# Optimization experiments

Hardware: AMD Instinct MI355X
Metric: run time of the kernel (lower is better)

## Reference

```python
import jax, jax.numpy as jnp
import numpy as np

B, S, H, D = 8, 1024, 16, 64
W = H * D  # hidden width = 1024


def setup_inputs() -> dict:
    key = jax.random.key(0)
    ks = jax.random.split(key, 5)
    std = 0.02
    return {
        "from_tensor": jax.random.normal(ks[0], (B, S, W), dtype=jnp.float32),
        "to_tensor": jax.random.normal(ks[1], (B, S, W), dtype=jnp.float32),
        "Wq": jax.random.normal(ks[2], (W, W), dtype=jnp.float32) * std,
        "bq": jnp.zeros((W,), dtype=jnp.float32),
        "Wk": jax.random.normal(ks[3], (W, W), dtype=jnp.float32) * std,
        "bk": jnp.zeros((W,), dtype=jnp.float32),
        "Wv": jax.random.normal(ks[4], (W, W), dtype=jnp.float32) * std,
        "bv": jnp.zeros((W,), dtype=jnp.float32),
    }


def reference(from_tensor, to_tensor, Wq, bq, Wk, bk, Wv, bv):
    # Q/K/V projections (no activations: query_act=key_act=value_act=None)
    q = from_tensor @ Wq + bq  # [B, S, W]
    k = to_tensor @ Wk + bk
    v = to_tensor @ Wv + bv
    # split heads -> [B, H, S, D]
    q = q.reshape(B, S, H, D).transpose(0, 2, 1, 3)
    k = k.reshape(B, S, H, D).transpose(0, 2, 1, 3)
    v = v.reshape(B, S, H, D).transpose(0, 2, 1, 3)
    scale = 1.0 / np.sqrt(float(D))
    scores = jnp.einsum("bhqd,bhkd->bhqk", q, k) * scale  # [B, H, S, S]
    # attention_mask=None, dropout_prob=0.0 -> no mask, no dropout
    probs = jax.nn.softmax(scores, axis=-1)
    ctx = jnp.einsum("bhqk,bhkd->bhqd", probs, v)  # [B, H, S, D]
    # merge heads -> [B, S, H*D] (do_return_2d_tensor=False)
    return ctx.transpose(0, 2, 1, 3).reshape(B, S, H * D)
```

## Files before the change

### kernel.cpp

```cpp
#include <hip/hip_runtime.h>
#include <hip/hip_bf16.h>
#include <math.h>


#define B_ 8
#define S_ 1024
#define H_ 16
#define D_ 64
#define W_ 1024

typedef __bf16 bf16x8 __attribute__((ext_vector_type(8)));
typedef float f32x4 __attribute__((ext_vector_type(4)));
typedef unsigned short ushort_t;

#define MFMA16(a, b, c) __builtin_amdgcn_mfma_f32_16x16x32_bf16((a), (b), (c), 0, 0, 0)

__device__ inline ushort_t f2bf(float f) {
    unsigned int u = __float_as_uint(f);
    u += 0x7fff + ((u >> 16) & 1);
    return (ushort_t)(u >> 16);
}

__device__ inline unsigned f2bf_rhu_u(float f) {
    return (__float_as_uint(f) + 0x8000u) >> 16;
}

__device__ inline void async16(const void* g, void* l) {
    __builtin_amdgcn_global_load_lds((const __attribute__((address_space(1))) void*)g,
                                     (__attribute__((address_space(3))) void*)l, 16, 0, 0);
}

__global__ __launch_bounds__(256) void cast2_bf16(const float* __restrict__ a,
                                                  const float* __restrict__ b,
                                                  ushort_t* __restrict__ da,
                                                  ushort_t* __restrict__ db, int n4) {
    int i = blockIdx.x * 256 + threadIdx.x;
    if (i >= n4) return;
    const float* src = blockIdx.y ? b : a;
    ushort_t* dst = blockIdx.y ? db : da;
    float4 v = ((const float4*)src)[i];
    ushort4 o;
    o.x = f2bf(v.x); o.y = f2bf(v.y); o.z = f2bf(v.z); o.w = f2bf(v.w);
    ((ushort4*)dst)[i] = o;
}

__global__ __launch_bounds__(256) void transpose_cast(const float* __restrict__ Wq,
                                                      const float* __restrict__ Wk,
                                                      const float* __restrict__ Wv,
                                                      ushort_t* __restrict__ Wt) {
    __shared__ float tile[32][33];
    int z = blockIdx.z;
    const float* src = (z == 0) ? Wq : (z == 1 ? Wk : Wv);
    ushort_t* dst = Wt + (size_t)z * W_ * W_;
    int tx = threadIdx.x, ty = threadIdx.y;
    int x = blockIdx.x * 32 + tx;
#pragma unroll
    for (int jj = 0; jj < 4; jj++) {
        int y = blockIdx.y * 32 + ty + jj * 8;
        tile[ty + jj * 8][tx] = src[(size_t)y * W_ + x];
    }
    __syncthreads();
    int x2 = blockIdx.y * 32 + tx;
#pragma unroll
    for (int jj = 0; jj < 4; jj++) {
        int y2 = blockIdx.x * 32 + ty + jj * 8;
        dst[(size_t)y2 * W_ + x2] = f2bf(tile[tx][ty + jj * 8]);
    }
}

__global__ __launch_bounds__(256) void qkv_gemm(const ushort_t* __restrict__ fromB,
                                                const ushort_t* __restrict__ toB,
                                                const ushort_t* __restrict__ Wt,
                                                const float* __restrict__ bq,
                                                const float* __restrict__ bk,
                                                const float* __restrict__ bv,
                                                ushort_t* __restrict__ Qd,
                                                ushort_t* __restrict__ Kd,
                                                ushort_t* __restrict__ Vt) {
    __shared__ __attribute__((aligned(16))) ushort_t As[128 * 32];
    __shared__ __attribute__((aligned(16))) ushort_t Bs[128 * 32];
    int z = blockIdx.y;
    const ushort_t* A = (z == 0) ? fromB : toB;
    const ushort_t* Bt = Wt + (size_t)z * (W_ * W_);
    const float* bias = (z == 0) ? bq : (z == 1 ? bk : bv);
    ushort_t* dst = (z == 0) ? Qd : (z == 1 ? Kd : Vt);

    int bx = blockIdx.x;
    int j64 = bx >> 3;
    int mTile = ((bx & 7) << 3) | (j64 >> 3);
    int nTile = j64 & 7;
    int mBase = mTile * 128, nBase = nTile * 128;

    int t = threadIdx.x;
    int lane = t & 63, w = t >> 6;
    int wm = w >> 1, wn = w & 1;
    int ln = lane & 15, qd = lane >> 4;
    int wb = t & ~63;
    int sG = ((t & 3) ^ ((t >> 3) & 3)) << 3;
    int fs = (qd ^ ((ln >> 1) & 3)) << 3;

    f32x4 zero = {0.f, 0.f, 0.f, 0.f};
    f32x4 acc[4][4];
#pragma unroll
    for (int i = 0; i < 4; i++)
#pragma unroll
        for (int j = 0; j < 4; j++) acc[i][j] = zero;

    for (int kt = 0; kt < 32; ++kt) {
        int k0 = kt * 32;
#pragma unroll
        for (int c = 0; c < 2; ++c) {
            int idx16 = c * 256 + t;
            int row = idx16 >> 2;
            async16(A + (size_t)(mBase + row) * W_ + k0 + sG, As + (size_t)(c * 256 + wb) * 8);
            async16(Bt + (size_t)(nBase + row) * W_ + k0 + sG, Bs + (size_t)(c * 256 + wb) * 8);
        }
        __syncthreads();
        bf16x8 af[4], bfr[4];
#pragma unroll
        for (int i = 0; i < 4; i++) af[i] = *(const bf16x8*)(As + (wm * 64 + i * 16 + ln) * 32 + fs);
#pragma unroll
        for (int j = 0; j < 4; j++) bfr[j] = *(const bf16x8*)(Bs + (wn * 64 + j * 16 + ln) * 32 + fs);
#pragma unroll
        for (int i = 0; i < 4; i++)
#pragma unroll
            for (int j = 0; j < 4; j++) acc[i][j] = MFMA16(af[i], bfr[j], acc[i][j]);
        __syncthreads();
    }

#pragma unroll
    for (int j = 0; j < 4; j++) {
        int n = nBase + wn * 64 + j * 16 + ln;
        float bb = bias[n];
        int h = n >> 6, d = n & 63;
#pragma unroll
        for (int i = 0; i < 4; i++) {
            int mrow = mBase + wm * 64 + i * 16 + qd * 4;
#pragma unroll
            for (int r = 0; r < 4; r++) {
                int m = mrow + r;
                int b = m >> 10, s = m & 1023;
                float v = acc[i][j][r] + bb;
                if (z == 0) v *= 0.18033688011111773f;
                size_t idx;
                if (z < 2) idx = ((size_t)(b * H_ + h) * S_ + s) * D_ + d;
                else       idx = ((size_t)(b * H_ + h) * D_ + d) * S_ + s;
                dst[idx] = f2bf(v);
            }
        }
    }
}

__global__ __launch_bounds__(256, 3) void attn(const ushort_t* __restrict__ Qd,
                                               const ushort_t* __restrict__ Kd,
                                               const ushort_t* __restrict__ Vt,
                                               float* __restrict__ out) {
    __shared__ __attribute__((aligned(16))) ushort_t Ks[2][4096];
    __shared__ __attribute__((aligned(16))) ushort_t Vs[2][4096];
    __shared__ __attribute__((aligned(16))) ushort_t Plds[4][32][72];

    int bh = blockIdx.y;
    int t = threadIdx.x, w = t >> 6, lane = t & 63;
    int ln = lane & 15, qd = lane >> 4;
    int qbase = blockIdx.x * 128 + w * 32;
    const ushort_t* Qb = Qd + (size_t)bh * S_ * D_;
    const ushort_t* Kb = Kd + (size_t)bh * S_ * D_;
    const ushort_t* Vb = Vt + (size_t)bh * D_ * S_;

    bf16x8 qf[2][2];
#pragma unroll
    for (int i = 0; i < 2; i++) {
        const ushort_t* qp = Qb + (size_t)(qbase + i * 16 + ln) * D_ + qd * 8;
        qf[i][0] = *(const bf16x8*)qp;
        qf[i][1] = *(const bf16x8*)(qp + 32);
    }

    int l8 = lane >> 3, s8 = lane & 7;
    int stgOff = (s8 ^ l8) << 3;
    const ushort_t* kg = Kb + (size_t)(w * 16 + l8) * D_ + stgOff;
    const ushort_t* vg = Vb + (size_t)(w * 16 + l8) * S_ + stgOff;
    int kOff = ln * 64 + ((qd ^ (ln & 7)) << 3);

    float rs[2] = {0.f, 0.f};
    f32x4 zero = {0.f, 0.f, 0.f, 0.f};
    f32x4 accO[2][4];
#pragma unroll
    for (int i = 0; i < 2; i++)
#pragma unroll
        for (int jd = 0; jd < 4; jd++) accO[i][jd] = zero;

    async16(kg, &Ks[0][w * 1024]);
    async16(kg + 8 * D_, &Ks[0][w * 1024 + 512]);
    async16(vg, &Vs[0][w * 1024]);
    async16(vg + 8 * S_, &Vs[0][w * 1024 + 512]);

    for (int c = 0; c < 16; ++c) {
        int buf = c & 1;
        __builtin_amdgcn_s_waitcnt(0x0F70);
        __syncthreads();
        if (c + 1 < 16) {
            int kc = (c + 1) * 64;
            async16(kg + (size_t)kc * D_, &Ks[buf ^ 1][w * 1024]);
            async16(kg + (size_t)kc * D_ + 8 * D_, &Ks[buf ^ 1][w * 1024 + 512]);
            async16(vg + kc, &Vs[buf ^ 1][w * 1024]);
            async16(vg + kc + 8 * S_, &Vs[buf ^ 1][w * 1024 + 512]);
        }

        f32x4 sc[2][4];
#pragma unroll
        for (int i = 0; i < 2; i++)
#pragma unroll
            for (int j = 0; j < 4; j++) sc[i][j] = zero;
        __builtin_amdgcn_s_setprio(1);
#pragma unroll
        for (int j = 0; j < 4; j++) {
            bf16x8 k0 = *(const bf16x8*)&Ks[buf][j * 1024 + kOff];
            bf16x8 k1 = *(const bf16x8*)&Ks[buf][(j * 1024 + kOff) ^ 32];
#pragma unroll
            for (int i = 0; i < 2; i++) {
                sc[i][j] = MFMA16(k0, qf[i][0], sc[i][j]);
                sc[i][j] = MFMA16(k1, qf[i][1], sc[i][j]);
            }
        }
        __builtin_amdgcn_s_setprio(0);
#pragma unroll
        for (int i = 0; i < 2; i++)
#pragma unroll
            for (int j = 0; j < 4; j++) {
                float p0 = exp2f(sc[i][j][0]);
                float p1 = exp2f(sc[i][j][1]);
                float p2 = exp2f(sc[i][j][2]);
                float p3 = exp2f(sc[i][j][3]);
                rs[i] += (p0 + p1) + (p2 + p3);
                uint2 pk;
                pk.x = f2bf_rhu_u(p0) | (f2bf_rhu_u(p1) << 16);
                pk.y = f2bf_rhu_u(p2) | (f2bf_rhu_u(p3) << 16);
                *(uint2*)&Plds[w][i * 16 + ln][j * 16 + qd * 4] = pk;
            }
        asm volatile("" ::: "memory");
        bf16x8 pf[2][2];
#pragma unroll
        for (int i = 0; i < 2; i++) {
            pf[i][0] = *(const bf16x8*)&Plds[w][i * 16 + ln][qd * 8];
            pf[i][1] = *(const bf16x8*)&Plds[w][i * 16 + ln][32 + qd * 8];
        }
        __builtin_amdgcn_s_setprio(1);
#pragma unroll
        for (int jd = 0; jd < 4; jd++) {
            bf16x8 v0 = *(const bf16x8*)&Vs[buf][jd * 1024 + kOff];
            bf16x8 v1 = *(const bf16x8*)&Vs[buf][(jd * 1024 + kOff) ^ 32];
#pragma unroll
            for (int i = 0; i < 2; i++) {
                accO[i][jd] = MFMA16(pf[i][0], v0, accO[i][jd]);
                accO[i][jd] = MFMA16(pf[i][1], v1, accO[i][jd]);
            }
        }
        __builtin_amdgcn_s_setprio(0);
    }

    float inv[2];
#pragma unroll
    for (int i = 0; i < 2; i++) {
        float s = rs[i];
        s += __shfl_xor(s, 16);
        s += __shfl_xor(s, 32);
        inv[i] = 1.f / s;
    }
    int b = bh >> 4, h = bh & 15;
#pragma unroll
    for (int i = 0; i < 2; i++)
#pragma unroll
        for (int r = 0; r < 4; r++) {
            float iv = __shfl(inv[i], qd * 4 + r);
            int q = qbase + i * 16 + qd * 4 + r;
            float* op = out + ((size_t)(b * S_ + q) * H_ + h) * D_;
#pragma unroll
            for (int jd = 0; jd < 4; jd++) op[jd * 16 + ln] = accO[i][jd][r] * iv;
        }
}

extern "C" void kernel_launch(void* const* d_in, const int* in_sizes, int n_in,
                              void* d_out, int out_size, void* d_ws, size_t ws_size,
                              hipStream_t stream) {
    const float* from = (const float*)d_in[0];
    const float* to_  = (const float*)d_in[1];
    const float* Wq = (const float*)d_in[2];
    const float* bq = (const float*)d_in[3];
    const float* Wk = (const float*)d_in[4];
    const float* bk = (const float*)d_in[5];
    const float* Wv = (const float*)d_in[6];
    const float* bv = (const float*)d_in[7];
    float* out = (float*)d_out;

    const size_t NTOK = (size_t)B_ * S_ * W_;
    ushort_t* ws = (ushort_t*)d_ws;
    ushort_t* fromB = ws;
    ushort_t* toB = fromB + NTOK;
    ushort_t* Wt = toB + NTOK;
    ushort_t* Qd = Wt + (size_t)3 * W_ * W_;
    ushort_t* Kd = Qd + NTOK;
    ushort_t* Vt = Kd + NTOK;

    int n4 = (int)(NTOK / 4);
    cast2_bf16<<<dim3(n4 / 256, 2), dim3(256), 0, stream>>>(from, to_, fromB, toB, n4);
    transpose_cast<<<dim3(32, 32, 3), dim3(32, 8), 0, stream>>>(Wq, Wk, Wv, Wt);
    qkv_gemm<<<dim3(512, 3), dim3(256), 0, stream>>>(fromB, toB, Wt, bq, bk, bv, Qd, Kd, Vt);
    attn<<<dim3(8, 128), dim3(256), 0, stream>>>(Qd, Kd, Vt, out);
}
```

Before: 273.0 us.

## Keep softmax probabilities in registers by permuting V layout, drop LDS round-trip

The projection epilogue now writes V with a permuted sequence index, so the P·V MFMA can take the exp'd score fragments straight from registers as the B operand instead of staging P through shared memory. This removes the per-iteration LDS write/read of P and the Plds buffer. The output store becomes float4-vectorized using the transposed accumulator layout. The GEMM's shared-memory XOR swizzle is also removed, which may reintroduce LDS bank conflicts. Correctness depends on the V permutation matching the attention kernel's V load indexing, and part of that indexing is not visible.

```diff
diff --git a/kernel.cpp b/kernel.cpp
--- a/kernel.cpp
+++ b/kernel.cpp
@@ -96,8 +96,6 @@
     int wm = w >> 1, wn = w & 1;
     int ln = lane & 15, qd = lane >> 4;
     int wb = t & ~63;
-    int sG = ((t & 3) ^ ((t >> 3) & 3)) << 3;
-    int fs = (qd ^ ((ln >> 1) & 3)) << 3;
 
     f32x4 zero = {0.f, 0.f, 0.f, 0.f};
     f32x4 acc[4][4];
@@ -111,16 +109,16 @@
 #pragma unroll
         for (int c = 0; c < 2; ++c) {
             int idx16 = c * 256 + t;
-            int row = idx16 >> 2;
-            async16(A + (size_t)(mBase + row) * W_ + k0 + sG, As + (size_t)(c * 256 + wb) * 8);
-            async16(Bt + (size_t)(nBase + row) * W_ + k0 + sG, Bs + (size_t)(c * 256 + wb) * 8);
+            int row = idx16 >> 2, seg = idx16 & 3;
+            async16(A + (size_t)(mBase + row) * W_ + k0 + seg * 8, As + (size_t)(c * 256 + wb) * 8);
+            async16(Bt + (size_t)(nBase + row) * W_ + k0 + seg * 8, Bs + (size_t)(c * 256 + wb) * 8);
         }
         __syncthreads();
         bf16x8 af[4], bfr[4];
 #pragma unroll
-        for (int i = 0; i < 4; i++) af[i] = *(const bf16x8*)(As + (wm * 64 + i * 16 + ln) * 32 + fs);
-#pragma unroll
-        for (int j = 0; j < 4; j++) bfr[j] = *(const bf16x8*)(Bs + (wn * 64 + j * 16 + ln) * 32 + fs);
+        for (int i = 0; i < 4; i++) af[i] = *(const bf16x8*)(As + (wm * 64 + i * 16 + ln) * 32 + qd * 8);
+#pragma unroll
+        for (int j = 0; j < 4; j++) bfr[j] = *(const bf16x8*)(Bs + (wn * 64 + j * 16 + ln) * 32 + qd * 8);
 #pragma unroll
         for (int i = 0; i < 4; i++)
 #pragma unroll
@@ -144,7 +142,10 @@
                 if (z == 0) v *= 0.18033688011111773f;
                 size_t idx;
                 if (z < 2) idx = ((size_t)(b * H_ + h) * S_ + s) * D_ + d;
-                else       idx = ((size_t)(b * H_ + h) * D_ + d) * S_ + s;
+                else {
+                    int sp = (s & ~63) | (s & 0x23) | ((s & 0x0C) << 1) | ((s & 0x10) >> 2);
+                    idx = ((size_t)(b * H_ + h) * D_ + d) * S_ + sp;
+                }
                 dst[idx] = f2bf(v);
             }
         }
@@ -157,7 +158,6 @@
                                                float* __restrict__ out) {
     __shared__ __attribute__((aligned(16))) ushort_t Ks[2][4096];
     __shared__ __attribute__((aligned(16))) ushort_t Vs[2][4096];
-    __shared__ __attribute__((aligned(16))) ushort_t Plds[4][32][72];
 
     int bh = blockIdx.y;
     int t = threadIdx.x, w = t >> 6, lane = t & 63;
@@ -223,38 +223,36 @@
             }
         }
         __builtin_amdgcn_s_setprio(0);
+
+        bf16x8 pfrag[2][2];
 #pragma unroll
         for (int i = 0; i < 2; i++)
 #pragma unroll
-            for (int j = 0; j < 4; j++) {
-                float p0 = exp2f(sc[i][j][0]);
-                float p1 = exp2f(sc[i][j][1]);
-                float p2 = exp2f(sc[i][j][2]);
-                float p3 = exp2f(sc[i][j][3]);
-                rs[i] += (p0 + p1) + (p2 + p3);
-                uint2 pk;
-                pk.x = f2bf_rhu_u(p0) | (f2bf_rhu_u(p1) << 16);
-                pk.y = f2bf_rhu_u(p2) | (f2bf_rhu_u(p3) << 16);
-                *(uint2*)&Plds[w][i * 16 + ln][j * 16 + qd * 4] = pk;
+            for (int m = 0; m < 2; m++) {
+                union { unsigned u[4]; bf16x8 v; } pk;
+#pragma unroll
+                for (int jh = 0; jh < 2; jh++) {
+                    float p0 = exp2f(sc[i][2 * m + jh][0]);
+                    float p1 = exp2f(sc[i][2 * m + jh][1]);
+                    float p2 = exp2f(sc[i][2 * m + jh][2]);
+                    float p3 = exp2f(sc[i][2 * m + jh][3]);
+                    rs[i] += (p0 + p1) + (p2 + p3);
+                    pk.u[jh * 2]     = f2bf_rhu_u(p0) | (f2bf_rhu_u(p1) << 16);
+                    pk.u[jh * 2 + 1] = f2bf_rhu_u(p2) | (f2bf_rhu_u(p3) << 16);
+                }
+                pfrag[i][m] = pk.v;
             }
-        asm volatile("" ::: "memory");
-        bf16x8 pf[2][2];
-#pragma unroll
-        for (int i = 0; i < 2; i++) {
-            pf[i][0] = *(const bf16x8*)&Plds[w][i * 16 + ln][qd * 8];
-            pf[i][1] = *(const bf16x8*)&Plds[w][i * 16 + ln][32 + qd * 8];
-        }
+
         __builtin_amdgcn_s_setprio(1);
 #pragma unroll
-        for (int jd = 0; jd < 4; jd++) {
-            bf16x8 v0 = *(const bf16x8*)&Vs[buf][jd * 1024 + kOff];
-            bf16x8 v1 = *(const bf16x8*)&Vs[buf][(jd * 1024 + kOff) ^ 32];
-#pragma unroll
-            for (int i = 0; i < 2; i++) {
-                accO[i][jd] = MFMA16(pf[i][0], v0, accO[i][jd]);
-                accO[i][jd] = MFMA16(pf[i][1], v1, accO[i][jd]);
+        for (int dt = 0; dt < 4; dt++)
+#pragma unroll
+            for (int m = 0; m < 2; m++) {
+                bf16x8 vf = *(const bf16x8*)&Vs[buf][(dt * 16 + ln) * 64 +
+                                                    ((((m << 2) + qd) ^ (ln & 7)) << 3)];
+                accO[0][dt] = MFMA16(vf, pfrag[0][m], accO[0][dt]);
+                accO[1][dt] = MFMA16(vf, pfrag[1][m], accO[1][dt]);
             }
-        }
         __builtin_amdgcn_s_setprio(0);
     }
 
@@ -268,15 +266,19 @@
     }
     int b = bh >> 4, h = bh & 15;
 #pragma unroll
-    for (int i = 0; i < 2; i++)
-#pragma unroll
-        for (int r = 0; r < 4; r++) {
-            float iv = __shfl(inv[i], qd * 4 + r);
-            int q = qbase + i * 16 + qd * 4 + r;
-            float* op = out + ((size_t)(b * S_ + q) * H_ + h) * D_;
-#pragma unroll
-            for (int jd = 0; jd < 4; jd++) op[jd * 16 + ln] = accO[i][jd][r] * iv;
-        }
+    for (int i = 0; i < 2; i++) {
+        int q = qbase + i * 16 + ln;
+        float* op = out + ((size_t)(b * S_ + q) * H_ + h) * D_ + qd * 4;
+#pragma unroll
+        for (int dt = 0; dt < 4; dt++) {
+            float4 o4;
+            o4.x = accO[i][dt][0] * inv[i];
+            o4.y = accO[i][dt][1] * inv[i];
+            o4.z = accO[i][dt][2] * inv[i];
+            o4.w = accO[i][dt][3] * inv[i];
+            *(float4*)(op + dt * 16) = o4;
+        }
+    }
 }
 
 extern "C" void kernel_launch(void* const* d_in, const int* in_sizes, int n_in,
```

After: 270.3 us. About the same (-1.0%).
